# Kernel tuning notes

Hardware: AMD Instinct MI355X
Metric: run time of the kernel (lower is better)

## Reference

```python
import jax, jax.numpy as jnp
import numpy as np

N = 50000; E = 800000; IN = 128; D = 256; H = 8; C = 32; L = 6; EPS = 1e-5

def setup_inputs() -> dict:
    key = jax.random.key(0)
    ks = jax.random.split(key, 16)
    r = lambda k, s: jax.random.normal(k, s, dtype=jnp.float32) * 0.1
    return {
        'x': jax.random.normal(ks[0], (N, IN), dtype=jnp.float32),
        'edge_index': jax.random.randint(ks[1], (2, E), 0, N, dtype=jnp.int32),
        'win_w': r(ks[2], (IN, D)), 'win_b': jnp.zeros((D,), jnp.float32),
        'bn1_g': jnp.ones((D,), jnp.float32), 'bn1_b': jnp.zeros((D,), jnp.float32),
        'ln_g': jnp.ones((L, D), jnp.float32), 'ln_b': jnp.zeros((L, D), jnp.float32),
        'Wl': r(ks[3], (L, D, D)), 'bl': jnp.zeros((L, D), jnp.float32),
        'Wr': r(ks[4], (L, D, D)), 'br': jnp.zeros((L, D), jnp.float32),
        'att': r(ks[5], (L, H, C)),
        'conv_b': jnp.zeros((L, D), jnp.float32),
        'scales': jnp.full((L,), 0.1, jnp.float32),
        'scale_weights': jnp.full((L,), 1.0 / L, jnp.float32),
        'h1_w': r(ks[6], (D, D)), 'h1_b': jnp.zeros((D,), jnp.float32),
        'bn2_g': jnp.ones((D,), jnp.float32), 'bn2_b': jnp.zeros((D,), jnp.float32),
        'h2_w': r(ks[7], (D, D // 2)), 'h2_b': jnp.zeros((D // 2,), jnp.float32),
        'h3_w': r(ks[8], (D // 2, 1)), 'h3_b': jnp.zeros((1,), jnp.float32),
    }

def _layernorm(x, g, b):
    mu = x.mean(-1, keepdims=True)
    var = ((x - mu) ** 2).mean(-1, keepdims=True)
    return (x - mu) / jnp.sqrt(var + EPS) * g + b

def _bn_eval(x, g, b):
    # BatchNorm1d in eval with default running stats (mean 0, var 1)
    return x / jnp.sqrt(1.0 + EPS) * g + b

def reference(x, edge_index, win_w, win_b, bn1_g, bn1_b, ln_g, ln_b, Wl, bl, Wr, br,
              att, conv_b, scales, scale_weights, h1_w, h1_b, bn2_g, bn2_b,
              h2_w, h2_b, h3_w, h3_b):
    n = x.shape[0]
    loop = jnp.arange(n, dtype=edge_index.dtype)
    src = jnp.concatenate([edge_index[0], loop])  # GATv2Conv adds self-loops
    dst = jnp.concatenate([edge_index[1], loop])

    h = jax.nn.leaky_relu(_bn_eval(x @ win_w + win_b, bn1_g, bn1_b), 0.1)

    outs = []
    for i in range(L):
        res = h
        hn = _layernorm(h, ln_g[i], ln_b[i])
        xl = (hn @ Wl[i] + bl[i]).reshape(n, H, C)  # source transform
        xr = (hn @ Wr[i] + br[i]).reshape(n, H, C)  # target transform
        e = jax.nn.leaky_relu(xl[src] + xr[dst], 0.2)            # [Etot,H,C]
        logit = jnp.einsum('ehc,hc->eh', e, att[i])              # [Etot,H]
        m = jax.ops.segment_max(logit, dst, num_segments=n)      # segment softmax
        ex = jnp.exp(logit - m[dst])
        den = jax.ops.segment_sum(ex, dst, num_segments=n)       # [N,H]
        agg = jax.ops.segment_sum(xl[src] * ex[:, :, None], dst, num_segments=n)
        o = (agg / den[:, :, None]).reshape(n, H * C) + conv_b[i]
        o = jax.nn.leaky_relu(o, 0.1)  # dropout skipped (eval)
        h = res + scales[i] * o
        outs.append(h)

    w = jax.nn.softmax(scale_weights)
    h = jnp.einsum('l,lnd->nd', w, jnp.stack(outs))

    y = jax.nn.leaky_relu(_bn_eval(h @ h1_w + h1_b, bn2_g, bn2_b), 0.1)
    y = jax.nn.leaky_relu(y @ h2_w + h2_b, 0.1)
    return y @ h3_w + h3_b
```

## Files before the change

kernel.cpp:

```cpp
#include <hip/hip_runtime.h>
#include <hip/hip_fp16.h>

#define NN 50000
#define EE 800000
#define LL 6
constexpr float EPSF = 1e-5f;

typedef _Float16 f16x8 __attribute__((ext_vector_type(8)));
typedef _Float16 f16x2 __attribute__((ext_vector_type(2)));
typedef float f32x4 __attribute__((ext_vector_type(4)));
typedef unsigned short u16x8 __attribute__((ext_vector_type(8)));

__device__ __forceinline__ float leaky(float v, float s) { return v > 0.f ? v : s * v; }

__device__ __forceinline__ f16x2 asf2(unsigned int u) {
    union { unsigned int u; f16x2 f; } x; x.u = u; return x.f;
}
__device__ __forceinline__ unsigned int asu2(f16x2 f) {
    union { f16x2 f; unsigned int u; } x; x.f = f; return x.u;
}
__device__ __forceinline__ f16x2 lrelu2_02(f16x2 v) {
    return __builtin_elementwise_max(v, v * (_Float16)0.2f);
}
__device__ __forceinline__ f16x2 pk2(float a, float b) {
    f16x2 r; r[0] = (_Float16)a; r[1] = (_Float16)b; return r;
}
__device__ __forceinline__ unsigned char f2fp8(float v) {
    return (unsigned char)(__builtin_amdgcn_cvt_pk_fp8_f32(v, v, 0, false) & 0xff);
}

#define GLD16(gp, sp) __builtin_amdgcn_global_load_lds( \
    (const __attribute__((address_space(1))) unsigned int*)(uintptr_t)(gp), \
    (__attribute__((address_space(3))) unsigned int*)(uintptr_t)(sp), 16, 0, 0)

__global__ __launch_bounds__(256) void prep_k(
    const float* __restrict__ win_w, const float* __restrict__ Wl,
    const float* __restrict__ Wr, const float* __restrict__ h1_w,
    const float* __restrict__ h2_w, const float* __restrict__ ln_g,
    const float* __restrict__ ln_b, const float* __restrict__ bl,
    const float* __restrict__ br, const float* __restrict__ att,
    const float* __restrict__ sw,
    __half* __restrict__ winT, __half* __restrict__ WlrT,
    __half* __restrict__ h1T, __half* __restrict__ h2T,
    __half* __restrict__ att_h, float* __restrict__ biasLR, float* __restrict__ wsm)
{
    __shared__ float t[64][65];
    const int bid = blockIdx.x, tid = threadIdx.x;
    if (bid < 224) {
        const float* in; __half* out; const float* gamma = nullptr;
        int K, N, kb, nb;
        if (bid < 8)        { in = win_w; out = winT; K = 128; N = 256; kb = bid >> 2; nb = bid & 3; }
        else if (bid < 104) { int i = bid - 8; int l = i >> 4, r = i & 15;
            in = Wl + (size_t)l * 65536; out = WlrT + (size_t)l * 131072;
            gamma = ln_g + l * 256; K = 256; N = 256; kb = r >> 2; nb = r & 3; }
        else if (bid < 200) { int i = bid - 104; int l = i >> 4, r = i & 15;
            in = Wr + (size_t)l * 65536; out = WlrT + (size_t)l * 131072 + 65536;
            gamma = ln_g + l * 256; K = 256; N = 256; kb = r >> 2; nb = r & 3; }
        else if (bid < 216) { int i = bid - 200; in = h1_w; out = h1T; K = 256; N = 256; kb = i >> 2; nb = i & 3; }
        else                { int i = bid - 216; in = h2_w; out = h2T; K = 256; N = 128; kb = i >> 1; nb = i & 1; }
        const int k0 = kb * 64, n0 = nb * 64;
        {
            int kl = tid >> 2, np = (tid & 3) * 16;
            const float* ip = in + (size_t)(k0 + kl) * N + n0 + np;
            float4 a = *(const float4*)(ip + 0);
            float4 b = *(const float4*)(ip + 4);
            float4 c = *(const float4*)(ip + 8);
            float4 d = *(const float4*)(ip + 12);
            t[kl][np + 0] = a.x; t[kl][np + 1] = a.y; t[kl][np + 2] = a.z; t[kl][np + 3] = a.w;
            t[kl][np + 4] = b.x; t[kl][np + 5] = b.y; t[kl][np + 6] = b.z; t[kl][np + 7] = b.w;
            t[kl][np + 8] = c.x; t[kl][np + 9] = c.y; t[kl][np +10] = c.z; t[kl][np +11] = c.w;
            t[kl][np +12] = d.x; t[kl][np +13] = d.y; t[kl][np +14] = d.z; t[kl][np +15] = d.w;
        }
        __syncthreads();
        {
            int nl = tid >> 2, kp = (tid & 3) * 16;
            u16x8 o0, o1;
#pragma unroll
            for (int i = 0; i < 8; ++i) {
                float g0 = gamma ? gamma[k0 + kp + i] : 1.f;
                float g1 = gamma ? gamma[k0 + kp + 8 + i] : 1.f;
                o0[i] = __half_as_ushort(__float2half(t[kp + i][nl] * g0));
                o1[i] = __half_as_ushort(__float2half(t[kp + 8 + i][nl] * g1));
            }
            unsigned short* op = (unsigned short*)out + (size_t)(n0 + nl) * K + k0 + kp;
            *(u16x8*)(op + 0) = o0;
            *(u16x8*)(op + 8) = o1;
        }
    } else if (bid < 236) {
        int i = bid - 224, l = i >> 1, side = i & 1, n = tid;
        const float* W = side ? Wr : Wl;
        const float* b = side ? br : bl;
        const float* lb = ln_b + l * 256;
        const float* Wp = W + (size_t)l * 65536;
        float acc = b[l * 256 + n];
        for (int k = 0; k < 256; ++k) acc = fmaf(lb[k], Wp[(size_t)k * 256 + n], acc);
        biasLR[l * 512 + side * 256 + n] = acc;
    } else if (bid < 242) {
        int l = bid - 236;
        att_h[l * 256 + tid] = __float2half(att[l * 256 + tid]);
    } else if (tid == 0) {
        float m = -1e30f;
        for (int l = 0; l < LL; ++l) m = fmaxf(m, sw[l]);
        float e[LL]; float s = 0.f;
        for (int l = 0; l < LL; ++l) { e[l] = __expf(sw[l] - m); s += e[l]; }
        float w[LL];
        for (int l = 0; l < LL; ++l) { w[l] = e[l] / s; wsm[l] = w[l]; }
        for (int l = 0; l < LL; ++l) {
            float S = 0.f;
            for (int k = l; k < LL; ++k) S += w[k];
            wsm[8 + l] = S;
        }
    }
}

__global__ __launch_bounds__(256) void cvt_h_k(const float* __restrict__ in,
                                               __half* __restrict__ out, int n)
{
    int i = blockIdx.x * 256 + threadIdx.x;
    if (i < n) out[i] = __float2half(in[i]);
}

template<int ACT, int OUT>
__global__ __launch_bounds__(256) void gemm_h_k(
    const __half* __restrict__ A, const __half* __restrict__ Bt,
    const float* __restrict__ bias, const float* __restrict__ g2,
    const float* __restrict__ b2, void* __restrict__ Cv,
    unsigned char* __restrict__ C8, __half* __restrict__ C16,
    int M, int K, int N)
{
    __shared__ _Float16 As[128 * 64];
    __shared__ _Float16 Bs[128 * 64];
    const int tid = threadIdx.x, lane = tid & 63, wave = tid >> 6;
    const int bm = blockIdx.x * 128, bn = blockIdx.y * 128;
    const int wm = (wave & 1) * 64, wn = (wave >> 1) * 64;
    const int mrow = lane & 15;
    const int sg = lane >> 3;
    const int sc = (lane & 7) ^ sg;

    f32x4 acc[4][4];
#pragma unroll
    for (int i = 0; i < 4; ++i)
#pragma unroll
        for (int j = 0; j < 4; ++j) acc[i][j] = (f32x4){0.f, 0.f, 0.f, 0.f};

    for (int k0 = 0; k0 < K; k0 += 64) {
#pragma unroll
        for (int t = 0; t < 4; ++t) {
            int R = 32 * wave + 8 * t;
            int ar = bm + R + sg; if (ar >= M) ar = M - 1;
            GLD16(A + (size_t)ar * K + k0 + sc * 8, &As[R * 64]);
        }
#pragma unroll
        for (int t = 0; t < 4; ++t) {
            int R = 32 * wave + 8 * t;
            GLD16(Bt + (size_t)(bn + R + sg) * K + k0 + sc * 8, &Bs[R * 64]);
        }
        __syncthreads();
#pragma unroll
        for (int s2 = 0; s2 < 2; ++s2) {
            const int c = s2 * 4 + (lane >> 4);
            f16x8 af[4], bf[4];
#pragma unroll
            for (int i = 0; i < 4; ++i) {
                int r = wm + 16 * i + mrow;
                af[i] = *(const f16x8*)&As[r * 64 + ((c ^ (r & 7)) * 8)];
            }
#pragma unroll
            for (int j = 0; j < 4; ++j) {
                int r = wn + 16 * j + mrow;
                bf[j] = *(const f16x8*)&Bs[r * 64 + ((c ^ (r & 7)) * 8)];
            }
#pragma unroll
            for (int i = 0; i < 4; ++i)
#pragma unroll
                for (int j = 0; j < 4; ++j)
                    acc[i][j] = __builtin_amdgcn_mfma_f32_16x16x32_f16(af[i], bf[j], acc[i][j], 0, 0, 0);
        }
        __syncthreads();
    }

    const float inv_s = 0.9999950000374997f;
    const int rq = (lane >> 4) * 4;
    float bsj[4], gj[4], bbj[4];
#pragma unroll
    for (int j = 0; j < 4; ++j) {
        int cc = bn + wn + 16 * j + mrow;
        bsj[j] = bias[cc];
        if constexpr (ACT == 1) { gj[j] = g2[cc]; bbj[j] = b2[cc]; }
    }
#pragma unroll
    for (int i = 0; i < 4; ++i)
#pragma unroll
        for (int r = 0; r < 4; ++r) {
            int grow = bm + wm + 16 * i + rq + r;
            if (grow >= M) continue;
#pragma unroll
            for (int j = 0; j < 4; ++j) {
                int cc = bn + wn + 16 * j + mrow;
                float v = acc[i][j][r] + bsj[j];
                if constexpr (ACT == 1) v = leaky(v * inv_s * gj[j] + bbj[j], 0.1f);
                else if constexpr (ACT == 2) v = leaky(v, 0.1f);
                if constexpr (OUT == 0)      ((float*)Cv)[(size_t)grow * N + cc] = v;
                else if constexpr (OUT == 1) ((__half*)Cv)[(size_t)grow * N + cc] = __float2half(v);
                else {
                    if (bn < 256) C8[(size_t)grow * 256 + cc] = f2fp8(v);
                    else          C16[(size_t)grow * 256 + (cc - 256)] = __float2half(v);
                }
            }
        }
}

__global__ __launch_bounds__(256) void ln_norm_k(const __half* __restrict__ h16,
                                                 __half* __restrict__ hacc,
                                                 __half* __restrict__ normed, int N)
{
    int wv = blockIdx.x * 4 + (threadIdx.x >> 6);
    if (wv >= N) return;
    int lane = threadIdx.x & 63;
    size_t off = (size_t)wv * 256 + lane * 4;
    uint2 u = *(const uint2*)((const unsigned short*)h16 + off);
    f16x2 p0 = asf2(u.x), p1 = asf2(u.y);
    float v0 = (float)p0[0], v1 = (float)p0[1], v2 = (float)p1[0], v3 = (float)p1[1];
    float s = v0 + v1 + v2 + v3;
#pragma unroll
    for (int o = 1; o < 64; o <<= 1) s += __shfl_xor(s, o);
    float m = s * (1.f / 256.f);
    float d0 = v0 - m, d1 = v1 - m, d2 = v2 - m, d3 = v3 - m;
    float q = d0 * d0 + d1 * d1 + d2 * d2 + d3 * d3;
#pragma unroll
    for (int o = 1; o < 64; o <<= 1) q += __shfl_xor(q, o);
    float rs = rsqrtf(q * (1.f / 256.f) + EPSF);
    *(uint2*)((unsigned short*)hacc + off) = u;
    uint2 o2;
    o2.x = asu2(pk2(d0 * rs, d1 * rs));
    o2.y = asu2(pk2(d2 * rs, d3 * rs));
    *(uint2*)((unsigned short*)normed + off) = o2;
}

__global__ __launch_bounds__(256) void hist_k(const int* __restrict__ ei, int E, int N,
                                              int* __restrict__ counts)
{
    int e = blockIdx.x * 256 + threadIdx.x;
    int Etot = E + N;
    if (e >= Etot) return;
    int d = (e < E) ? ei[E + e] : (e - E);
    atomicAdd(&counts[d], 1);
}

__global__ __launch_bounds__(256) void scanA_k(const int* __restrict__ counts,
                                               int* __restrict__ bsum, int N)
{
    int i = blockIdx.x * 256 + threadIdx.x;
    int v = (i < N) ? counts[i] : 0;
    int s = v;
#pragma unroll
    for (int o = 1; o < 64; o <<= 1) s += __shfl_xor(s, o);
    __shared__ int ws[4];
    if ((threadIdx.x & 63) == 0) ws[threadIdx.x >> 6] = s;
    __syncthreads();
    if (threadIdx.x == 0) bsum[blockIdx.x] = ws[0] + ws[1] + ws[2] + ws[3];
}

__global__ __launch_bounds__(256) void scanB_k(const int* __restrict__ bsum,
                                               int* __restrict__ bpre, int nb)
{
    int t = threadIdx.x;
    int v = (t < nb) ? bsum[t] : 0;
    int lane = t & 63, w = t >> 6;
    int incl = v;
#pragma unroll
    for (int o = 1; o < 64; o <<= 1) { int u = __shfl_up(incl, o); if (lane >= o) incl += u; }
    __shared__ int ws[4];
    if (lane == 63) ws[w] = incl;
    __syncthreads();
    if (t == 0) { int run = 0; for (int k = 0; k < 4; ++k) { int x = ws[k]; ws[k] = run; run += x; } }
    __syncthreads();
    if (t < nb) bpre[t] = ws[w] + incl - v;
}

__global__ __launch_bounds__(256) void scanC_k(int* __restrict__ counts,
                                               const int* __restrict__ bpre,
                                               int* __restrict__ offsets, int N, int Etot)
{
    int i = blockIdx.x * 256 + threadIdx.x;
    int v = (i < N) ? counts[i] : 0;
    int lane = threadIdx.x & 63, w = threadIdx.x >> 6;
    int incl = v;
#pragma unroll
    for (int o = 1; o < 64; o <<= 1) { int u = __shfl_up(incl, o); if (lane >= o) incl += u; }
    __shared__ int ws[4];
    if (lane == 63) ws[w] = incl;
    __syncthreads();
    if (threadIdx.x == 0) { int run = 0; for (int k = 0; k < 4; ++k) { int x = ws[k]; ws[k] = run; run += x; } }
    __syncthreads();
    int ex = bpre[blockIdx.x] + ws[w] + incl - v;
    if (i < N) { offsets[i] = ex; counts[i] = ex; }
    if (i == 0) offsets[N] = Etot;
}

__global__ __launch_bounds__(256) void scatter_k(const int* __restrict__ ei, int E, int N,
                                                 int* __restrict__ cursor, int* __restrict__ eidx)
{
    int e = blockIdx.x * 256 + threadIdx.x;
    int Etot = E + N;
    if (e >= Etot) return;
    int s, d;
    if (e < E) { s = ei[e]; d = ei[E + e]; }
    else       { s = e - E; d = s; }
    int pos = atomicAdd(&cursor[d], 1);
    eidx[pos] = s;
}

__global__ __launch_bounds__(256) void edge_k(
    const unsigned char* __restrict__ xl8, const __half* __restrict__ xr16,
    const __half* __restrict__ atth, const float* __restrict__ convb,
    const int* __restrict__ offsets, const int* __restrict__ eidx,
    __half* __restrict__ h16, __half* __restrict__ hacc,
    __half* __restrict__ normed,
    const float* __restrict__ wsm, const float* __restrict__ scales,
    int layer, int N)
{
    int wv = blockIdx.x * 4 + (threadIdx.x >> 6);
    if (wv >= N) return;
    const int lane = threadIdx.x & 63;
    const int slot = lane >> 4, sl = lane & 15;
    const int c0 = sl * 16;

    f16x2 atv[8], xrv[8];
    {
        const unsigned short* ap = (const unsigned short*)atth + c0;
        const unsigned short* xp = (const unsigned short*)xr16 + (size_t)wv * 256 + c0;
        uint4 a0 = *(const uint4*)ap, a1 = *(const uint4*)(ap + 8);
        uint4 x0 = *(const uint4*)xp, x1 = *(const uint4*)(xp + 8);
        atv[0]=asf2(a0.x); atv[1]=asf2(a0.y); atv[2]=asf2(a0.z); atv[3]=asf2(a0.w);
        atv[4]=asf2(a1.x); atv[5]=asf2(a1.y); atv[6]=asf2(a1.z); atv[7]=asf2(a1.w);
        xrv[0]=asf2(x0.x); xrv[1]=asf2(x0.y); xrv[2]=asf2(x0.z); xrv[3]=asf2(x0.w);
        xrv[4]=asf2(x1.x); xrv[5]=asf2(x1.y); xrv[6]=asf2(x1.z); xrv[7]=asf2(x1.w);
    }
    const int e0 = offsets[wv], e1 = offsets[wv + 1], e1m = e1 - 1;
    f16x2 a2[8];
#pragma unroll
    for (int p = 0; p < 8; ++p) a2[p] = pk2(0.f, 0.f);
    float den = 0.f;

    for (int base = e0; base < e1; base += 4) {
        int e = base + slot;
        bool v = e < e1;
        int s = eidx[v ? e : e1m];
        uint4 w = *(const uint4*)(xl8 + (size_t)s * 256 + c0);
        f16x2 xv[8];
        xv[0] = __builtin_amdgcn_cvt_scalef32_pk_f16_fp8(w.x, 1.0f, false);
        xv[1] = __builtin_amdgcn_cvt_scalef32_pk_f16_fp8(w.x, 1.0f, true);
        xv[2] = __builtin_amdgcn_cvt_scalef32_pk_f16_fp8(w.y, 1.0f, false);
        xv[3] = __builtin_amdgcn_cvt_scalef32_pk_f16_fp8(w.y, 1.0f, true);
        xv[4] = __builtin_amdgcn_cvt_scalef32_pk_f16_fp8(w.z, 1.0f, false);
        xv[5] = __builtin_amdgcn_cvt_scalef32_pk_f16_fp8(w.z, 1.0f, true);
        xv[6] = __builtin_amdgcn_cvt_scalef32_pk_f16_fp8(w.w, 1.0f, false);
        xv[7] = __builtin_amdgcn_cvt_scalef32_pk_f16_fp8(w.w, 1.0f, true);
        float pm = 0.f;
#pragma unroll
        for (int p = 0; p < 8; ++p) {
            f16x2 t = lrelu2_02(xv[p] + xrv[p]);
            pm = __builtin_amdgcn_fdot2(t, atv[p], pm, false);
        }
        pm += __shfl_xor(pm, 1);
        float exf = v ? __expf(pm) : 0.f;
        den += exf;
        _Float16 eh = (_Float16)exf;
        f16x2 e2; e2[0] = eh; e2[1] = eh;
#pragma unroll
        for (int p = 0; p < 8; ++p) a2[p] += xv[p] * e2;
    }

    den += __shfl_xor(den, 16); den += __shfl_xor(den, 32);
#pragma unroll
    for (int p = 0; p < 8; ++p) {
        a2[p] += asf2((unsigned int)__shfl_xor((int)asu2(a2[p]), 16));
        a2[p] += asf2((unsigned int)__shfl_xor((int)asu2(a2[p]), 32));
    }

    const int p0 = 2 * slot;
    const float inv = 1.f / den;
    const float sc = scales[layer], Sl = wsm[8 + layer];
    const int cc = c0 + 4 * slot;
    const size_t rb = (size_t)wv * 256 + cc;
    float4 cb = *(const float4*)(convb + cc);
    uint2 hu = *(const uint2*)((const unsigned short*)h16 + rb);
    f16x2 h0 = asf2(hu.x), h1 = asf2(hu.y);
    float d00 = sc * leaky(fmaf((float)a2[p0][0],     inv, cb.x), 0.1f);
    float d01 = sc * leaky(fmaf((float)a2[p0][1],     inv, cb.y), 0.1f);
    float d10 = sc * leaky(fmaf((float)a2[p0 + 1][0], inv, cb.z), 0.1f);
    float d11 = sc * leaky(fmaf((float)a2[p0 + 1][1], inv, cb.w), 0.1f);
    float hn0 = (float)h0[0] + d00, hn1 = (float)h0[1] + d01;
    float hn2 = (float)h1[0] + d10, hn3 = (float)h1[1] + d11;

    {
        uint2 au = *(const uint2*)((const unsigned short*)hacc + rb);
        f16x2 A0 = asf2(au.x), A1 = asf2(au.y);
        uint2 ao;
        ao.x = asu2(pk2(fmaf(Sl, d00, (float)A0[0]), fmaf(Sl, d01, (float)A0[1])));
        ao.y = asu2(pk2(fmaf(Sl, d10, (float)A1[0]), fmaf(Sl, d11, (float)A1[1])));
        *(uint2*)((unsigned short*)hacc + rb) = ao;
    }

    if (layer != LL - 1) {
        uint2 ho;
        ho.x = asu2(pk2(hn0, hn1));
        ho.y = asu2(pk2(hn2, hn3));
        *(uint2*)((unsigned short*)h16 + rb) = ho;
        float s1 = hn0 + hn1 + hn2 + hn3;
#pragma unroll
        for (int o = 1; o < 64; o <<= 1) s1 += __shfl_xor(s1, o);
        float m = s1 * (1.f / 256.f);
        float dd0 = hn0 - m, dd1 = hn1 - m, dd2 = hn2 - m, dd3 = hn3 - m;
        float qv = dd0 * dd0 + dd1 * dd1 + dd2 * dd2 + dd3 * dd3;
#pragma unroll
        for (int o = 1; o < 64; o <<= 1) qv += __shfl_xor(qv, o);
        float rs = rsqrtf(qv * (1.f / 256.f) + EPSF);
        uint2 no;
        no.x = asu2(pk2(dd0 * rs, dd1 * rs));
        no.y = asu2(pk2(dd2 * rs, dd3 * rs));
        *(uint2*)((unsigned short*)normed + rb) = no;
    }
}

__global__ __launch_bounds__(256) void out_k(const float* __restrict__ y2,
                                             const float* __restrict__ w,
                                             const float* __restrict__ b,
                                             float* __restrict__ out, int N)
{
    int wv = blockIdx.x * 4 + (threadIdx.x >> 6);
    if (wv >= N) return;
    int lane = threadIdx.x & 63;
    float2 v = *(const float2*)(y2 + (size_t)wv * 128 + lane * 2);
    float2 ww = *(const float2*)(w + lane * 2);
    float pm = v.x * ww.x + v.y * ww.y;
#pragma unroll
    for (int off = 1; off < 64; off <<= 1) pm += __shfl_xor(pm, off);
    if (lane == 0) out[wv] = pm + b[0];
}

extern "C" void kernel_launch(void* const* d_in, const int* in_sizes, int n_in,
                              void* d_out, int out_size, void* d_ws, size_t ws_size,
                              hipStream_t stream)
{
    const int N = NN, E = EE, Etot = EE + NN;
    const float* x      = (const float*)d_in[0];
    const int*   ei     = (const int*)  d_in[1];
    const float* win_w  = (const float*)d_in[2];
    const float* win_b  = (const float*)d_in[3];
    const float* bn1_g  = (const float*)d_in[4];
    const float* bn1_b  = (const float*)d_in[5];
    const float* ln_g   = (const float*)d_in[6];
    const float* ln_b   = (const float*)d_in[7];
    const float* Wl     = (const float*)d_in[8];
    const float* bl     = (const float*)d_in[9];
    const float* Wr     = (const float*)d_in[10];
    const float* br     = (const float*)d_in[11];
    const float* att    = (const float*)d_in[12];
    const float* conv_b = (const float*)d_in[13];
    const float* scales = (const float*)d_in[14];
    const float* sw     = (const float*)d_in[15];
    const float* h1_w   = (const float*)d_in[16];
    const float* h1_b   = (const float*)d_in[17];
    const float* bn2_g  = (const float*)d_in[18];
    const float* bn2_b  = (const float*)d_in[19];
    const float* h2_w   = (const float*)d_in[20];
    const float* h2_b   = (const float*)d_in[21];
    const float* h3_w   = (const float*)d_in[22];
    const float* h3_b   = (const float*)d_in[23];

    char* p = (char*)d_ws;
    auto take = [&](size_t b) -> char* {
        char* q = p; p += (b + 255) & ~(size_t)255; return q;
    };
    __half* h16     = (__half*)take((size_t)N * 256 * 2);
    __half* hacc    = (__half*)take((size_t)N * 256 * 2);
    __half* norm    = (__half*)take((size_t)N * 256 * 2);
    unsigned char* xl8 = (unsigned char*)take((size_t)N * 256);
    __half* xr16    = (__half*)take((size_t)N * 256 * 2);
    __half* xh      = (__half*)take((size_t)N * 128 * 2);
    float*  y2      = (float*)take((size_t)N * 128 * 4);
    float* wsm      = (float*)take(256);
    int*   offsets  = (int*)take((size_t)(N + 1) * 4);
    int*   cursor   = (int*)take((size_t)N * 4);
    int*   eidx     = (int*)take((size_t)Etot * 4);
    int*   bsum     = (int*)take(256 * 4);
    int*   bpre     = (int*)take(256 * 4);
    __half* winT    = (__half*)take((size_t)256 * 128 * 2);
    __half* WlrT    = (__half*)take((size_t)LL * 512 * 256 * 2);
    __half* h1T     = (__half*)take((size_t)256 * 256 * 2);
    __half* h2T     = (__half*)take((size_t)128 * 256 * 2);
    __half* att_h   = (__half*)take((size_t)LL * 256 * 2);
    float* biasLR   = (float*)take((size_t)LL * 512 * 4);
    __half* y1b = xr16;

    const int EB = (Etot + 255) / 256;
    const int NB = (N + 3) / 4;
    const int SB = (N + 255) / 256;

    hipMemsetAsync(cursor, 0, (size_t)N * 4, stream);
    hist_k<<<EB, 256, 0, stream>>>(ei, E, N, cursor);
    scanA_k<<<SB, 256, 0, stream>>>(cursor, bsum, N);
    scanB_k<<<1, 256, 0, stream>>>(bsum, bpre, SB);
    scanC_k<<<SB, 256, 0, stream>>>(cursor, bpre, offsets, N, Etot);
    scatter_k<<<EB, 256, 0, stream>>>(ei, E, N, cursor, eidx);

    prep_k<<<243, 256, 0, stream>>>(win_w, Wl, Wr, h1_w, h2_w, ln_g, ln_b, bl, br, att, sw,
                                    winT, WlrT, h1T, h2T, att_h, biasLR, wsm);
    cvt_h_k<<<(N * 128 + 255) / 256, 256, 0, stream>>>(x, xh, N * 128);

    dim3 g2d((N + 127) / 128, 2);
    dim3 g4d((N + 127) / 128, 4);

    gemm_h_k<1, 1><<<g2d, 256, 0, stream>>>(xh, winT, win_b, bn1_g, bn1_b, h16,
                                            nullptr, nullptr, N, 128, 256);
    ln_norm_k<<<NB, 256, 0, stream>>>(h16, hacc, norm, N);

    for (int l = 0; l < LL; ++l) {
        gemm_h_k<0, 2><<<g4d, 256, 0, stream>>>(norm, WlrT + (size_t)l * 131072,
                                                biasLR + l * 512, nullptr, nullptr,
                                                nullptr, xl8, xr16, N, 256, 512);
        edge_k<<<NB, 256, 0, stream>>>(xl8, xr16, att_h + l * 256, conv_b + l * 256,
                                       offsets, eidx, h16, hacc, norm,
                                       wsm, scales, l, N);
    }

    gemm_h_k<1, 1><<<g2d, 256, 0, stream>>>(hacc, h1T, h1_b, bn2_g, bn2_b, y1b,
                                            nullptr, nullptr, N, 256, 256);
    gemm_h_k<2, 0><<<dim3((N + 127) / 128, 1), 256, 0, stream>>>(
        y1b, h2T, h2_b, nullptr, nullptr, y2, nullptr, nullptr, N, 256, 128);
    out_k<<<NB, 256, 0, stream>>>(y2, h3_w, h3_b, (float*)d_out, N);
}
```

Baseline: 921.4 us.

## Fold LayerNorm into GEMM epilogue via per-row stats and weight column sums

```diff
diff --git a/kernel.cpp b/kernel.cpp
--- a/kernel.cpp
+++ b/kernel.cpp
@@ -42,7 +42,8 @@
     const float* __restrict__ sw,
     __half* __restrict__ winT, __half* __restrict__ WlrT,
     __half* __restrict__ h1T, __half* __restrict__ h2T,
-    __half* __restrict__ att_h, float* __restrict__ biasLR, float* __restrict__ wsm)
+    __half* __restrict__ att_h, float* __restrict__ biasLR,
+    float* __restrict__ colsumLR, float* __restrict__ wsm)
 {
     __shared__ float t[64][65];
     const int bid = blockIdx.x, tid = threadIdx.x;
@@ -91,10 +92,17 @@
         const float* W = side ? Wr : Wl;
         const float* b = side ? br : bl;
         const float* lb = ln_b + l * 256;
+        const float* lg = ln_g + l * 256;
         const float* Wp = W + (size_t)l * 65536;
-        float acc = b[l * 256 + n];
-        for (int k = 0; k < 256; ++k) acc = fmaf(lb[k], Wp[(size_t)k * 256 + n], acc);
-        biasLR[l * 512 + side * 256 + n] = acc;
+        float accb = b[l * 256 + n];
+        float accc = 0.f;
+        for (int k = 0; k < 256; ++k) {
+            float wv = Wp[(size_t)k * 256 + n];
+            accb = fmaf(lb[k], wv, accb);
+            accc = fmaf(lg[k], wv, accc);
+        }
+        biasLR[l * 512 + side * 256 + n] = accb;
+        colsumLR[l * 512 + side * 256 + n] = accc;
     } else if (bid < 242) {
         int l = bid - 236;
         att_h[l * 256 + tid] = __float2half(att[l * 256 + tid]);
@@ -124,8 +132,10 @@
 __global__ __launch_bounds__(256) void gemm_h_k(
     const __half* __restrict__ A, const __half* __restrict__ Bt,
     const float* __restrict__ bias, const float* __restrict__ g2,
-    const float* __restrict__ b2, void* __restrict__ Cv,
-    unsigned char* __restrict__ C8, __half* __restrict__ C16,
+    const float* __restrict__ b2,
+    const float* __restrict__ mu, const float* __restrict__ rsig,
+    const float* __restrict__ colsum,
+    void* __restrict__ Cv, unsigned char* __restrict__ C8, __half* __restrict__ C16,
     int M, int K, int N)
 {
     __shared__ _Float16 As[128 * 64];
@@ -181,12 +191,13 @@
 
     const float inv_s = 0.9999950000374997f;
     const int rq = (lane >> 4) * 4;
-    float bsj[4], gj[4], bbj[4];
+    float bsj[4], gj[4], bbj[4], csj[4];
 #pragma unroll
     for (int j = 0; j < 4; ++j) {
         int cc = bn + wn + 16 * j + mrow;
         bsj[j] = bias[cc];
         if constexpr (ACT == 1) { gj[j] = g2[cc]; bbj[j] = b2[cc]; }
+        if constexpr (ACT == 3) { csj[j] = colsum[cc]; }
     }
 #pragma unroll
     for (int i = 0; i < 4; ++i)
@@ -194,10 +205,14 @@
         for (int r = 0; r < 4; ++r) {
             int grow = bm + wm + 16 * i + rq + r;
             if (grow >= M) continue;
+            float rsv = 0.f, rmu = 0.f;
+            if constexpr (ACT == 3) { rsv = rsig[grow]; rmu = rsv * mu[grow]; }
 #pragma unroll
             for (int j = 0; j < 4; ++j) {
                 int cc = bn + wn + 16 * j + mrow;
-                float v = acc[i][j][r] + bsj[j];
+                float v;
+                if constexpr (ACT == 3) v = fmaf(rsv, acc[i][j][r], fmaf(-rmu, csj[j], bsj[j]));
+                else v = acc[i][j][r] + bsj[j];
                 if constexpr (ACT == 1) v = leaky(v * inv_s * gj[j] + bbj[j], 0.1f);
                 else if constexpr (ACT == 2) v = leaky(v, 0.1f);
                 if constexpr (OUT == 0)      ((float*)Cv)[(size_t)grow * N + cc] = v;
@@ -210,9 +225,10 @@
         }
 }
 
-__global__ __launch_bounds__(256) void ln_norm_k(const __half* __restrict__ h16,
-                                                 __half* __restrict__ hacc,
-                                                 __half* __restrict__ normed, int N)
+__global__ __launch_bounds__(256) void ln_stats_k(const __half* __restrict__ h16,
+                                                  __half* __restrict__ hacc,
+                                                  float* __restrict__ mu,
+                                                  float* __restrict__ rsig, int N)
 {
     int wv = blockIdx.x * 4 + (threadIdx.x >> 6);
     if (wv >= N) return;
@@ -231,10 +247,7 @@
     for (int o = 1; o < 64; o <<= 1) q += __shfl_xor(q, o);
     float rs = rsqrtf(q * (1.f / 256.f) + EPSF);
     *(uint2*)((unsigned short*)hacc + off) = u;
-    uint2 o2;
-    o2.x = asu2(pk2(d0 * rs, d1 * rs));
-    o2.y = asu2(pk2(d2 * rs, d3 * rs));
-    *(uint2*)((unsigned short*)normed + off) = o2;
+    if (lane == 0) { mu[wv] = m; rsig[wv] = rs; }
 }
 
 __global__ __launch_bounds__(256) void hist_k(const int* __restrict__ ei, int E, int N,
@@ -316,7 +329,7 @@
     const __half* __restrict__ atth, const float* __restrict__ convb,
     const int* __restrict__ offsets, const int* __restrict__ eidx,
     __half* __restrict__ h16, __half* __restrict__ hacc,
-    __half* __restrict__ normed,
+    float* __restrict__ mu, float* __restrict__ rsig,
     const float* __restrict__ wsm, const float* __restrict__ scales,
     int layer, int N)
 {
@@ -417,10 +430,7 @@
 #pragma unroll
         for (int o = 1; o < 64; o <<= 1) qv += __shfl_xor(qv, o);
         float rs = rsqrtf(qv * (1.f / 256.f) + EPSF);
-        uint2 no;
-        no.x = asu2(pk2(dd0 * rs, dd1 * rs));
-        no.y = asu2(pk2(dd2 * rs, dd3 * rs));
-        *(uint2*)((unsigned short*)normed + rb) = no;
+        if (lane == 0) { mu[wv] = m; rsig[wv] = rs; }
     }
 }
 
@@ -476,7 +486,8 @@
     };
     __half* h16     = (__half*)take((size_t)N * 256 * 2);
     __half* hacc    = (__half*)take((size_t)N * 256 * 2);
-    __half* norm    = (__half*)take((size_t)N * 256 * 2);
+    float*  mu      = (float*)take((size_t)N * 4);
+    float*  rsig    = (float*)take((size_t)N * 4);
     unsigned char* xl8 = (unsigned char*)take((size_t)N * 256);
     __half* xr16    = (__half*)take((size_t)N * 256 * 2);
     __half* xh      = (__half*)take((size_t)N * 128 * 2);
@@ -493,6 +504,7 @@
     __half* h2T     = (__half*)take((size_t)128 * 256 * 2);
     __half* att_h   = (__half*)take((size_t)LL * 256 * 2);
     float* biasLR   = (float*)take((size_t)LL * 512 * 4);
+    float* colsumLR = (float*)take((size_t)LL * 512 * 4);
     __half* y1b = xr16;
 
     const int EB = (Etot + 255) / 256;
@@ -507,28 +519,32 @@
     scatter_k<<<EB, 256, 0, stream>>>(ei, E, N, cursor, eidx);
 
     prep_k<<<243, 256, 0, stream>>>(win_w, Wl, Wr, h1_w, h2_w, ln_g, ln_b, bl, br, att, sw,
-                                    winT, WlrT, h1T, h2T, att_h, biasLR, wsm);
+                                    winT, WlrT, h1T, h2T, att_h, biasLR, colsumLR, wsm);
     cvt_h_k<<<(N * 128 + 255) / 256, 256, 0, stream>>>(x, xh, N * 128);
 
     dim3 g2d((N + 127) / 128, 2);
     dim3 g4d((N + 127) / 128, 4);
 
-    gemm_h_k<1, 1><<<g2d, 256, 0, stream>>>(xh, winT, win_b, bn1_g, bn1_b, h16,
-                                            nullptr, nullptr, N, 128, 256);
-    ln_norm_k<<<NB, 256, 0, stream>>>(h16, hacc, norm, N);
+    gemm_h_k<1, 1><<<g2d, 256, 0, stream>>>(xh, winT, win_b, bn1_g, bn1_b,
+                                            nullptr, nullptr, nullptr,
+                                            h16, nullptr, nullptr, N, 128, 256);
+    ln_stats_k<<<NB, 256, 0, stream>>>(h16, hacc, mu, rsig, N);
 
     for (int l = 0; l < LL; ++l) {
-        gemm_h_k<0, 2><<<g4d, 256, 0, stream>>>(norm, WlrT + (size_t)l * 131072,
+        gemm_h_k<3, 2><<<g4d, 256, 0, stream>>>(h16, WlrT + (size_t)l * 131072,
                                                 biasLR + l * 512, nullptr, nullptr,
+                                                mu, rsig, colsumLR + l * 512,
                                                 nullptr, xl8, xr16, N, 256, 512);
         edge_k<<<NB, 256, 0, stream>>>(xl8, xr16, att_h + l * 256, conv_b + l * 256,
-                                       offsets, eidx, h16, hacc, norm,
+                                       offsets, eidx, h16, hacc, mu, rsig,
                                        wsm, scales, l, N);
     }
 
-    gemm_h_k<1, 1><<<g2d, 256, 0, stream>>>(hacc, h1T, h1_b, bn2_g, bn2_b, y1b,
-                                            nullptr, nullptr, N, 256, 256);
+    gemm_h_k<1, 1><<<g2d, 256, 0, stream>>>(hacc, h1T, h1_b, bn2_g, bn2_b,
+                                            nullptr, nullptr, nullptr,
+                                            y1b, nullptr, nullptr, N, 256, 256);
     gemm_h_k<2, 0><<<dim3((N + 127) / 128, 1), 256, 0, stream>>>(
-        y1b, h2T, h2_b, nullptr, nullptr, y2, nullptr, nullptr, N, 256, 128);
+        y1b, h2T, h2_b, nullptr, nullptr, nullptr, nullptr, nullptr,
+        y2, nullptr, nullptr, N, 256, 128);
     out_k<<<NB, 256, 0, stream>>>(y2, h3_w, h3_b, (float*)d_out, N);
 }
```

Result: slower. 945.6 us (+2.6%).
